# Optimization experiments

Measured on AMD Instinct MI355X. Metric: run time of the kernel, lower is better.

## Reference

```python
import jax, jax.numpy as jnp
import numpy as np

D_EMBED = 2048
N_HEAD = 16
HEAD_DIM = D_EMBED // N_HEAD
B, S = 4, 2048


def setup_inputs() -> dict:
    key = jax.random.key(0)
    ks = jax.random.split(key, 6)
    s = 0.02
    x = jax.random.normal(ks[0], (B, S, D_EMBED), dtype=jnp.float32)
    attention_mask = jnp.ones((B, S), dtype=bool)
    Wq = jax.random.normal(ks[1], (D_EMBED, D_EMBED), dtype=jnp.float32) * s
    Wk = jax.random.normal(ks[2], (D_EMBED, D_EMBED), dtype=jnp.float32) * s
    Wv = jax.random.normal(ks[3], (D_EMBED, D_EMBED), dtype=jnp.float32) * s
    Wo = jax.random.normal(ks[4], (D_EMBED, D_EMBED), dtype=jnp.float32) * s
    bq = jnp.zeros((D_EMBED,), jnp.float32)
    bk = jnp.zeros((D_EMBED,), jnp.float32)
    bv = jnp.zeros((D_EMBED,), jnp.float32)
    bo = jnp.zeros((D_EMBED,), jnp.float32)
    return {"x": x, "attention_mask": attention_mask,
            "Wq": Wq, "bq": bq, "Wk": Wk, "bk": bk,
            "Wv": Wv, "bv": bv, "Wo": Wo, "bo": bo}


def reference(x, attention_mask, Wq, bq, Wk, bk, Wv, bv, Wo, bo):
    bsz, seq_len, _ = x.shape

    def split_heads(t):  # [B,S,D] -> [B,H,S,hd]
        return t.reshape(bsz, seq_len, N_HEAD, HEAD_DIM).transpose(0, 2, 1, 3)

    q = split_heads(x @ Wq + bq)
    k = split_heads(x @ Wk + bk)
    v = split_heads(x @ Wv + bv)

    scale = 1.0 / np.sqrt(HEAD_DIM).astype(np.float32)
    scores = jnp.einsum('bhqd,bhkd->bhqk', q, k) * scale  # [B,H,S,S]

    # causal (past_len = 0, query_len = total_len = S) combined with key padding mask
    causal = jnp.tril(jnp.ones((seq_len, seq_len), dtype=bool))  # [S,S]
    mask = causal[None, None, :, :] & attention_mask[:, None, None, :]
    neg = jnp.finfo(scores.dtype).min
    scores = jnp.where(mask, scores, neg)

    att = jax.nn.softmax(scores, axis=-1)  # dropout p=0.0 -> identity
    out = jnp.einsum('bhqk,bhkd->bhqd', att, v)
    out = out.transpose(0, 2, 1, 3).reshape(bsz, seq_len, D_EMBED)
    return out @ Wo + bo
```

## Files before the change

kernel.cpp:

```cpp
#include <hip/hip_runtime.h>
#include <cstdint>
#include <cstddef>


#define D_EMBED 2048
#define NHEAD   16
#define HDIM    128
#define BATCH   4
#define SEQ     2048
#define MROWS   (BATCH*SEQ)

typedef __attribute__((ext_vector_type(8))) short bf16x8;
typedef __attribute__((ext_vector_type(4))) float f32x4;

__device__ __forceinline__ short f2bf(float f) {
  union { float f; uint32_t u; } v; v.f = f;
  uint32_t r = v.u + 0x7fffu + ((v.u >> 16) & 1u);
  return (short)(r >> 16);
}

__device__ __forceinline__ void async_copy16(void* lds, const void* gmem) {
  __builtin_amdgcn_global_load_lds(
      (__attribute__((address_space(1))) void*)gmem,
      (__attribute__((address_space(3))) void*)lds, 16, 0, 0);
}

__global__ __launch_bounds__(256) void cvt_x(const float* __restrict__ x,
                                             short* __restrict__ xb) {
  int i = blockIdx.x * 256 + threadIdx.x;
  float4 v = reinterpret_cast<const float4*>(x)[i];
  short4 o;
  o.x = f2bf(v.x); o.y = f2bf(v.y); o.z = f2bf(v.z); o.w = f2bf(v.w);
  reinterpret_cast<short4*>(xb)[i] = o;
}

struct TransArgs { const float* src[4]; short* dst[4]; };

__global__ __launch_bounds__(256) void transpose_w(TransArgs ta) {
  const int z = blockIdx.z;
  const float* W = ta.src[z];
  short* Wt = ta.dst[z];
  __shared__ float tile[32][33];
  int bx = blockIdx.x * 32, by = blockIdx.y * 32;
  int tx = threadIdx.x & 31, ty = threadIdx.x >> 5;
#pragma unroll
  for (int r = ty; r < 32; r += 8)
    tile[r][tx] = W[(size_t)(by + r) * D_EMBED + bx + tx];
  __syncthreads();
#pragma unroll
  for (int r = ty; r < 32; r += 8)
    Wt[(size_t)(bx + r) * D_EMBED + by + tx] = f2bf(tile[tx][r]);
}

struct GemmArgs {
  const short* A;
  const short* Bt[3];
  const float* bias[3];
  void*        out[3];
  float        scale[3];
  int          mode[3];
};

__global__ __launch_bounds__(512, 2) void gemm256(GemmArgs ga) {
  const int z = blockIdx.z;
  const short* __restrict__ A  = ga.A;
  const short* __restrict__ Bt = ga.Bt[z];

  const int lin  = blockIdx.y * 8 + blockIdx.x;
  const int wg   = (lin & 7) * 32 + (lin >> 3);
  const int col0 = (wg & 7) * 256;
  const int row0 = (wg >> 3) * 256;

  __shared__ __align__(16) short As[2][2][2][64 * 64];
  __shared__ __align__(16) short Bs[2][2][128 * 64];

  const int tid  = threadIdx.x;
  const int lane = tid & 63, w = tid >> 6;
  const int lr   = lane & 15, quad = lane >> 4;
  const int wm   = w >> 2, wn = w & 3;
  const int lr8  = lane >> 3;
  const int srccol = ((lane & 7) ^ ((lane >> 3) & 7)) * 8;
  const int csw = (quad ^ (lr & 7)) * 8;

  bf16x8 av[4][2], bva[2][2], bvb[2][2];
  f32x4 acc[8][4] = {};

#define STAGE_A(buf, Mh, kk) do {                                              \
    _Pragma("unroll")                                                          \
    for (int j = 0; j < 2; ++j)                                                \
      async_copy16(&As[buf][Mh][j][w * 512],                                   \
          A + (size_t)(row0 + j * 128 + (Mh) * 64 + w * 8 + lr8) * D_EMBED +   \
              (kk) + srccol);                                                  \
  } while (0)

#define STAGE_B(buf, Nh, kk) do {                                              \
    _Pragma("unroll")                                                          \
    for (int j = 0; j < 2; ++j) {                                              \
      int fr_ = j * 64 + w * 8 + lr8;                                          \
      async_copy16(&Bs[buf][Nh][(j * 64 + w * 8) * 64],                        \
          Bt + (size_t)(col0 + (fr_ >> 5) * 64 + (Nh) * 32 + (fr_ & 31)) *     \
                  D_EMBED + (kk) + srccol);                                    \
    }                                                                          \
  } while (0)

#define LOAD_A(buf, Mh) do {                                                   \
    _Pragma("unroll")                                                          \
    for (int t = 0; t < 4; ++t) {                                              \
      const short* ap_ = &As[buf][Mh][wm][(t * 16 + lr) * 64];                 \
      av[t][0] = *reinterpret_cast<const bf16x8*>(ap_ + csw);                  \
      av[t][1] = *reinterpret_cast<const bf16x8*>(ap_ + (csw ^ 32));           \
    }                                                                          \
  } while (0)

#define LOAD_B(buf, Nh, dst) do {                                              \
    _Pragma("unroll")                                                          \
    for (int u = 0; u < 2; ++u) {                                              \
      const short* bp_ = &Bs[buf][Nh][(wn * 32 + u * 16 + lr) * 64];           \
      dst[u][0] = *reinterpret_cast<const bf16x8*>(bp_ + csw);                 \
      dst[u][1] = *reinterpret_cast<const bf16x8*>(bp_ + (csw ^ 32));          \
    }                                                                          \
  } while (0)

#define MFMA_Q(Mh, Nh, bv) do {                                                \
    _Pragma("unroll")                                                          \
    for (int ks = 0; ks < 2; ++ks)                                             \
      _Pragma("unroll")                                                        \
      for (int t = 0; t < 4; ++t)                                              \
        _Pragma("unroll")                                                      \
        for (int u = 0; u < 2; ++u)                                            \
          acc[(Mh) * 4 + t][(Nh) * 2 + u] =                                    \
              __builtin_amdgcn_mfma_f32_16x16x32_bf16(                         \
                  av[t][ks], bv[u][ks], acc[(Mh) * 4 + t][(Nh) * 2 + u],       \
                  0, 0, 0);                                                    \
  } while (0)

#define PHASE_TAIL(Mh, Nh, bv) do {                                            \
    __builtin_amdgcn_s_barrier();                                              \
    asm volatile("s_waitcnt lgkmcnt(0)" ::: "memory");                         \
    __builtin_amdgcn_sched_barrier(0);                                         \
    __builtin_amdgcn_s_setprio(1);                                             \
    MFMA_Q(Mh, Nh, bv);                                                        \
    __builtin_amdgcn_s_setprio(0);                                             \
    __builtin_amdgcn_s_barrier();                                              \
  } while (0)

#define PHASE_TAIL_NOLOAD(Mh, Nh, bv) do {                                     \
    __builtin_amdgcn_s_barrier();                                              \
    __builtin_amdgcn_s_setprio(1);                                             \
    MFMA_Q(Mh, Nh, bv);                                                        \
    __builtin_amdgcn_s_setprio(0);                                             \
    __builtin_amdgcn_s_barrier();                                              \
  } while (0)

  STAGE_A(0, 0, 0);  STAGE_B(0, 1, 0);  STAGE_A(0, 1, 0);  STAGE_B(0, 0, 0);
  STAGE_A(1, 0, 64); STAGE_B(1, 1, 64); STAGE_A(1, 1, 64);
  asm volatile("s_waitcnt vmcnt(6)" ::: "memory");
  __builtin_amdgcn_s_barrier();

#pragma unroll 1
  for (int it = 0; it < 16; ++it) {
    const int kc = it * 128;
    LOAD_A(0, 0); LOAD_B(0, 0, bva);
    STAGE_B(1, 0, kc + 64);
    asm volatile("s_waitcnt lgkmcnt(8)" ::: "memory");
    PHASE_TAIL(0, 0, bva);
    LOAD_B(0, 1, bvb);
    STAGE_A(0, 0, kc + 128);
    PHASE_TAIL(0, 1, bvb);
    LOAD_A(0, 1);
    STAGE_B(0, 1, kc + 128);
    PHASE_TAIL(1, 1, bvb);
    STAGE_A(0, 1, kc + 128);
    asm volatile("s_waitcnt vmcnt(6)" ::: "memory");
    PHASE_TAIL_NOLOAD(1, 0, bva);
    LOAD_A(1, 0); LOAD_B(1, 0, bva);
    STAGE_B(0, 0, kc + 128);
    asm volatile("s_waitcnt lgkmcnt(8)" ::: "memory");
    PHASE_TAIL(0, 0, bva);
    LOAD_B(1, 1, bvb);
    STAGE_A(1, 0, kc + 192);
    PHASE_TAIL(0, 1, bvb);
    LOAD_A(1, 1);
    STAGE_B(1, 1, kc + 192);
    PHASE_TAIL(1, 1, bvb);
    STAGE_A(1, 1, kc + 192);
    asm volatile("s_waitcnt vmcnt(6)" ::: "memory");
    PHASE_TAIL_NOLOAD(1, 0, bva);
  }
  asm volatile("s_waitcnt vmcnt(0)" ::: "memory");

#undef STAGE_A
#undef STAGE_B
#undef LOAD_A
#undef LOAD_B
#undef MFMA_Q
#undef PHASE_TAIL
#undef PHASE_TAIL_NOLOAD

  const float* __restrict__ bias = ga.bias[z];
  const int mode = ga.mode[z];
  const float scl = ga.scale[z];
  if (mode != 2) {
#pragma unroll
    for (int mi = 0; mi < 8; ++mi)
#pragma unroll
      for (int ni = 0; ni < 4; ++ni) {
        int n = col0 + wn * 64 + ni * 16 + lr;
        float bias_n = bias[n];
#pragma unroll
        for (int i = 0; i < 4; ++i) {
          int m = row0 + wm * 128 + mi * 16 + quad * 4 + i;
          float v = (acc[mi][ni][i] + bias_n) * scl;
          if (mode == 0) ((short*)ga.out[z])[(size_t)m * D_EMBED + n] = f2bf(v);
          else           ((float*)ga.out[z])[(size_t)m * D_EMBED + n] = v;
        }
      }
  } else {
    short* Vt = (short*)ga.out[z];
#pragma unroll
    for (int ni = 0; ni < 4; ++ni) {
      int n = col0 + wn * 64 + ni * 16 + lr;
      int h = n >> 7, dd = n & (HDIM - 1);
      float bias_n = bias[n];
#pragma unroll
      for (int mi = 0; mi < 8; ++mi)
#pragma unroll
        for (int i = 0; i < 4; ++i) {
          int m = row0 + wm * 128 + mi * 16 + quad * 4 + i;
          int b = m >> 11, t = m & (SEQ - 1);
          Vt[(size_t)((b * NHEAD + h) * HDIM + dd) * SEQ + t] = f2bf(acc[mi][ni][i] + bias_n);
        }
    }
  }
}

#define COMPUTE_STRIP(Kp, Vp, qf, o, l_i, qrow, diag, t0)                       \
  {                                                                             \
    f32x4 sc[4] = {};                                                           \
    __builtin_amdgcn_s_setprio(1);                                              \
    _Pragma("unroll")                                                           \
    for (int nt = 0; nt < 4; ++nt)                                              \
      _Pragma("unroll")                                                         \
      for (int ks = 0; ks < 4; ++ks) {                                          \
        bf16x8 kf = *reinterpret_cast<const bf16x8*>(                           \
            &(Kp)[(nt * 16 + lr) * 128 + (((ks * 4 + quad) ^ lr) * 8)]);        \
        sc[nt] = __builtin_amdgcn_mfma_f32_16x16x32_bf16(qf[ks], kf, sc[nt], 0, 0, 0); \
      }                                                                         \
    __builtin_amdgcn_s_setprio(0);                                              \
    if (diag) {                                                                 \
      _Pragma("unroll")                                                         \
      for (int nt = 0; nt < 4; ++nt) {                                          \
        int t = (t0) + nt * 16 + lr;                                            \
        _Pragma("unroll")                                                       \
        for (int i = 0; i < 4; ++i)                                             \
          if (t > (qrow) + quad * 4 + i) sc[nt][i] = -1e30f;                    \
      }                                                                         \
    }                                                                           \
    _Pragma("unroll")                                                           \
    for (int nt = 0; nt < 4; ++nt)                                              \
      _Pragma("unroll")                                                         \
      for (int i = 0; i < 4; ++i) {                                             \
        float p = exp2f(sc[nt][i]);                                             \
        l_i[i] += p;                                                            \
        Pls[wave][(quad * 4 + i) * 72 + nt * 16 + lr] = f2bf(p);                \
      }                                                                         \
    __builtin_amdgcn_s_setprio(1);                                              \
    _Pragma("unroll")                                                           \
    for (int n2 = 0; n2 < 8; ++n2)                                              \
      _Pragma("unroll")                                                         \
      for (int k2 = 0; k2 < 2; ++k2) {                                          \
        bf16x8 pf = *reinterpret_cast<const bf16x8*>(                           \
            &Pls[wave][lr * 72 + k2 * 32 + quad * 8]);                          \
        bf16x8 vf = *reinterpret_cast<const bf16x8*>(                           \
            &(Vp)[(n2 * 16 + lr) * 64 + (((k2 * 4 + quad) ^ (lr & 7)) * 8)]);   \
        o[n2] = __builtin_amdgcn_mfma_f32_16x16x32_bf16(pf, vf, o[n2], 0, 0, 0);\
      }                                                                         \
    __builtin_amdgcn_s_setprio(0);                                              \
  }

#define FINALIZE_STRIP(o, l_i, qrow)                                            \
  {                                                                             \
    _Pragma("unroll")                                                           \
    for (int off = 1; off < 16; off <<= 1)                                      \
      _Pragma("unroll")                                                         \
      for (int i = 0; i < 4; ++i) l_i[i] += __shfl_xor(l_i[i], off);            \
    float inv_l[4];                                                             \
    _Pragma("unroll")                                                           \
    for (int i = 0; i < 4; ++i) inv_l[i] = 1.0f / l_i[i];                       \
    short* obase = O + (size_t)(b * SEQ + (qrow)) * D_EMBED + h * HDIM;         \
    _Pragma("unroll")                                                           \
    for (int n2 = 0; n2 < 8; ++n2)                                              \
      _Pragma("unroll")                                                         \
      for (int i = 0; i < 4; ++i)                                               \
        obase[(size_t)(quad * 4 + i) * D_EMBED + n2 * 16 + lr] =                \
            f2bf(o[n2][i] * inv_l[i]);                                          \
  }

#define STAGE_KV(cb, tbase)                                                     \
  {                                                                             \
    _Pragma("unroll")                                                           \
    for (int s = 0; s < 4; ++s) {                                               \
      int r0 = wave * 16 + s * 4;                                               \
      int r  = r0 + krow;                                                       \
      int cg = (kcg_base ^ ((s * 4 + krow) & 15)) * 8;                          \
      async_copy16(&Kls[cb][r0 * 128],                                          \
                   Kbase + (size_t)((tbase) + r) * D_EMBED + cg);               \
    }                                                                           \
    _Pragma("unroll")                                                           \
    for (int s = 0; s < 4; ++s) {                                               \
      int r0 = wave * 32 + s * 8;                                               \
      int r  = r0 + vrow;                                                       \
      async_copy16(&Vls[cb][r0 * 64],                                           \
                   Vtbase + (size_t)r * SEQ + (tbase) + vcg);                   \
    }                                                                           \
  }

__global__ __launch_bounds__(256, 2) void flash_attn(const short* __restrict__ Q,
                                                     const short* __restrict__ K,
                                                     const short* __restrict__ Vt,
                                                     short* __restrict__ O) {
  __shared__ short Kls[2][64 * 128];
  __shared__ short Vls[2][128 * 64];
  __shared__ short Pls[4][16 * 72];

  const int lane = threadIdx.x & 63, wave = threadIdx.x >> 6;
  const int lr = lane & 15, quad = lane >> 4;
  const int b = blockIdx.z, h = blockIdx.y;
  const int qb_lo = blockIdx.x;
  const int qb_hi = 31 - qb_lo;
  const int qrow_lo = qb_lo * 64 + wave * 16;
  const int qrow_hi = qb_hi * 64 + wave * 16;

  const int krow = lane >> 4;
  const int kcg_base = lane & 15;
  const int vrow = lane >> 3;
  const int vcg = ((lane & 7) ^ (lane >> 3)) * 8;

  bf16x8 qf_lo[4], qf_hi[4];
  {
    const short* qp0 = Q + (size_t)(b * SEQ + qrow_lo + lr) * D_EMBED + h * HDIM;
    const short* qp1 = Q + (size_t)(b * SEQ + qrow_hi + lr) * D_EMBED + h * HDIM;
#pragma unroll
    for (int ks = 0; ks < 4; ++ks) {
      qf_lo[ks] = *reinterpret_cast<const bf16x8*>(qp0 + ks * 32 + quad * 8);
      qf_hi[ks] = *reinterpret_cast<const bf16x8*>(qp1 + ks * 32 + quad * 8);
    }
  }

  f32x4 o_lo[8] = {}, o_hi[8] = {};
  float l_lo[4] = {}, l_hi[4] = {};

  const short* Kbase  = K + (size_t)b * SEQ * D_EMBED + h * HDIM;
  const short* Vtbase = Vt + (size_t)((b * NHEAD + h) * HDIM) * SEQ;

  STAGE_KV(0, 0);
  __syncthreads();

  int cur = 0;
  for (int tt = 0; tt <= qb_hi; ++tt) {
    const int t0 = tt * 64;
    if (tt < qb_hi) STAGE_KV(cur ^ 1, t0 + 64);
    const short* Kp = &Kls[cur][0];
    const short* Vp = &Vls[cur][0];

    COMPUTE_STRIP(Kp, Vp, qf_hi, o_hi, l_hi, qrow_hi, tt == qb_hi, t0);
    if (tt <= qb_lo)
      COMPUTE_STRIP(Kp, Vp, qf_lo, o_lo, l_lo, qrow_lo, tt == qb_lo, t0);

    __syncthreads();
    cur ^= 1;
  }

  FINALIZE_STRIP(o_hi, l_hi, qrow_hi);
  FINALIZE_STRIP(o_lo, l_lo, qrow_lo);
}

extern "C" void kernel_launch(void* const* d_in, const int* in_sizes, int n_in,
                              void* d_out, int out_size, void* d_ws, size_t ws_size,
                              hipStream_t stream) {
  const float* x  = (const float*)d_in[0];
  const float* Wq = (const float*)d_in[2];
  const float* bq = (const float*)d_in[3];
  const float* Wk = (const float*)d_in[4];
  const float* bk = (const float*)d_in[5];
  const float* Wv = (const float*)d_in[6];
  const float* bv = (const float*)d_in[7];
  const float* Wo = (const float*)d_in[8];
  const float* bo = (const float*)d_in[9];

  char* ws = (char*)d_ws;
  const size_t MB32 = (size_t)MROWS * D_EMBED * 2;
  const size_t WSZ  = (size_t)D_EMBED * D_EMBED * 2;
  short* Xb   = (short*)(ws);
  short* Wqt  = (short*)(ws + MB32);
  short* Wkt  = (short*)(ws + MB32 + WSZ);
  short* Wvt  = (short*)(ws + MB32 + 2 * WSZ);
  short* Wot  = (short*)(ws + MB32 + 3 * WSZ);
  short* Qb   = (short*)(ws + 2 * MB32);
  short* Kb   = (short*)(ws + 3 * MB32);
  short* Vtb  = (short*)(ws + 4 * MB32);
  short* attn = Xb;

  const float scale2 = 0.08838834764831845f * 1.4426950408889634f;

  cvt_x<<<(MROWS * D_EMBED) / 4 / 256, 256, 0, stream>>>(x, Xb);

  TransArgs ta{{Wq, Wk, Wv, Wo}, {Wqt, Wkt, Wvt, Wot}};
  transpose_w<<<dim3(64, 64, 4), 256, 0, stream>>>(ta);

  GemmArgs ga;
  ga.A = Xb;
  ga.Bt[0] = Wqt; ga.Bt[1] = Wkt; ga.Bt[2] = Wvt;
  ga.bias[0] = bq; ga.bias[1] = bk; ga.bias[2] = bv;
  ga.out[0] = Qb; ga.out[1] = Kb; ga.out[2] = Vtb;
  ga.scale[0] = scale2; ga.scale[1] = 1.f; ga.scale[2] = 1.f;
  ga.mode[0] = 0; ga.mode[1] = 0; ga.mode[2] = 2;
  gemm256<<<dim3(D_EMBED / 256, MROWS / 256, 3), 512, 0, stream>>>(ga);

  flash_attn<<<dim3(16, NHEAD, BATCH), 256, 0, stream>>>(Qb, Kb, Vtb, attn);

  GemmArgs gb;
  gb.A = attn;
  gb.Bt[0] = Wot; gb.Bt[1] = Wot; gb.Bt[2] = Wot;
  gb.bias[0] = bo; gb.bias[1] = bo; gb.bias[2] = bo;
  gb.out[0] = d_out; gb.out[1] = d_out; gb.out[2] = d_out;
  gb.scale[0] = 1.f; gb.scale[1] = 1.f; gb.scale[2] = 1.f;
  gb.mode[0] = 1; gb.mode[1] = 1; gb.mode[2] = 1;
  gemm256<<<dim3(D_EMBED / 256, MROWS / 256, 1), 512, 0, stream>>>(gb);
}
```

Baseline: 576.9 us.

## Restructure GEMM main loop to prefetch LDS fragments one phase ahead with fewer barriers

Reworks the software pipeline of the projection GEMM main loop. LDS fragment loads for B are now issued one phase ahead and ping-pong between bva/bvb. Each phase uses a single barrier instead of two, and the explicit lgkmcnt waits and sched_barrier are dropped. This is meant to overlap LDS reads and global-to-LDS staging with MFMA work and cut synchronization stalls. It relies on the compiler inserting correct lgkmcnt waits, and it changes the staging order and vmcnt thresholds, which risks LDS read/write hazards if the ordering is wrong.

```diff
diff --git a/kernel.cpp b/kernel.cpp
--- a/kernel.cpp
+++ b/kernel.cpp
@@ -134,58 +134,44 @@
                   0, 0, 0);                                                    \
   } while (0)
 
-#define PHASE_TAIL(Mh, Nh, bv) do {                                            \
-    __builtin_amdgcn_s_barrier();                                              \
-    asm volatile("s_waitcnt lgkmcnt(0)" ::: "memory");                         \
-    __builtin_amdgcn_sched_barrier(0);                                         \
+#define PHASE(Mh, Nh, bv) do {                                                 \
     __builtin_amdgcn_s_setprio(1);                                             \
     MFMA_Q(Mh, Nh, bv);                                                        \
     __builtin_amdgcn_s_setprio(0);                                             \
     __builtin_amdgcn_s_barrier();                                              \
   } while (0)
 
-#define PHASE_TAIL_NOLOAD(Mh, Nh, bv) do {                                     \
-    __builtin_amdgcn_s_barrier();                                              \
-    __builtin_amdgcn_s_setprio(1);                                             \
-    MFMA_Q(Mh, Nh, bv);                                                        \
-    __builtin_amdgcn_s_setprio(0);                                             \
-    __builtin_amdgcn_s_barrier();                                              \
-  } while (0)
-
-  STAGE_A(0, 0, 0);  STAGE_B(0, 1, 0);  STAGE_A(0, 1, 0);  STAGE_B(0, 0, 0);
-  STAGE_A(1, 0, 64); STAGE_B(1, 1, 64); STAGE_A(1, 1, 64);
-  asm volatile("s_waitcnt vmcnt(6)" ::: "memory");
+  STAGE_A(0, 0, 0);  STAGE_B(0, 0, 0);  STAGE_B(0, 1, 0);  STAGE_A(0, 1, 0);
+  STAGE_A(1, 0, 64); STAGE_B(1, 0, 64); STAGE_B(1, 1, 64); STAGE_A(1, 1, 64);
+  asm volatile("s_waitcnt vmcnt(0)" ::: "memory");
   __builtin_amdgcn_s_barrier();
+  LOAD_B(0, 0, bva);
 
 #pragma unroll 1
   for (int it = 0; it < 16; ++it) {
     const int kc = it * 128;
-    LOAD_A(0, 0); LOAD_B(0, 0, bva);
-    STAGE_B(1, 0, kc + 64);
-    asm volatile("s_waitcnt lgkmcnt(8)" ::: "memory");
-    PHASE_TAIL(0, 0, bva);
-    LOAD_B(0, 1, bvb);
-    STAGE_A(0, 0, kc + 128);
-    PHASE_TAIL(0, 1, bvb);
+    LOAD_A(0, 0); LOAD_B(0, 1, bvb);
+    PHASE(0, 0, bva);
+    STAGE_A(0, 0, kc + 128); STAGE_B(0, 0, kc + 128);
+    PHASE(0, 1, bvb);
     LOAD_A(0, 1);
     STAGE_B(0, 1, kc + 128);
-    PHASE_TAIL(1, 1, bvb);
+    PHASE(1, 1, bvb);
+    LOAD_B(1, 0, bvb);
     STAGE_A(0, 1, kc + 128);
-    asm volatile("s_waitcnt vmcnt(6)" ::: "memory");
-    PHASE_TAIL_NOLOAD(1, 0, bva);
-    LOAD_A(1, 0); LOAD_B(1, 0, bva);
-    STAGE_B(0, 0, kc + 128);
-    asm volatile("s_waitcnt lgkmcnt(8)" ::: "memory");
-    PHASE_TAIL(0, 0, bva);
-    LOAD_B(1, 1, bvb);
-    STAGE_A(1, 0, kc + 192);
-    PHASE_TAIL(0, 1, bvb);
+    asm volatile("s_waitcnt vmcnt(4)" ::: "memory");
+    PHASE(1, 0, bva);
+    LOAD_A(1, 0); LOAD_B(1, 1, bva);
+    PHASE(0, 0, bvb);
+    STAGE_B(1, 0, kc + 192); STAGE_A(1, 0, kc + 192);
+    PHASE(0, 1, bva);
     LOAD_A(1, 1);
     STAGE_B(1, 1, kc + 192);
-    PHASE_TAIL(1, 1, bvb);
+    PHASE(1, 1, bva);
+    LOAD_B(0, 0, bva);
     STAGE_A(1, 1, kc + 192);
-    asm volatile("s_waitcnt vmcnt(6)" ::: "memory");
-    PHASE_TAIL_NOLOAD(1, 0, bva);
+    asm volatile("s_waitcnt vmcnt(4)" ::: "memory");
+    PHASE(1, 0, bvb);
   }
   asm volatile("s_waitcnt vmcnt(0)" ::: "memory");
 
@@ -194,8 +180,7 @@
 #undef LOAD_A
 #undef LOAD_B
 #undef MFMA_Q
-#undef PHASE_TAIL
-#undef PHASE_TAIL_NOLOAD
+#undef PHASE
 
   const float* __restrict__ bias = ga.bias[z];
   const int mode = ga.mode[z];
```

Measured after the change: 583.2 us. About the same (+1.1%).
